# Kernel tuning notes

Measured on AMD Instinct MI355X. Metric: run time of the kernel, lower is better.

The kernel has to match this reference:

```python
import jax, jax.numpy as jnp
import numpy as np

B, T, D, H, K = 4, 2048, 512, 8, 31
INNER = 2048  # dim * ff_mult
DH = D // H   # 64
EPS = 1e-5

def _ln(x, g, b):
    m = jnp.mean(x, axis=-1, keepdims=True)
    v = jnp.var(x, axis=-1, keepdims=True)
    return (x - m) * jax.lax.rsqrt(v + EPS) * g + b

def _ff(x, g, b, w1, b1, w2, b2):
    h = jax.nn.silu(_ln(x, g, b) @ w1 + b1)
    return h @ w2 + b2

def _rope_cos_sin(t, dh, theta=10000.0):
    freqs = 1.0 / theta ** (jnp.arange(0, dh, 2, dtype=jnp.float32) / dh)
    ang = jnp.arange(t, dtype=jnp.float32)[:, None] * freqs[None, :]
    return jnp.cos(ang), jnp.sin(ang)

def _rotate(x, cos, sin):
    # x: [B,T,H,DH]; complex rotation on (even, odd) pairs, matches torch view_as_complex
    xr = x.reshape(x.shape[:-1] + (DH // 2, 2))
    xe, xo = xr[..., 0], xr[..., 1]
    c, s = cos[None, :, None, :], sin[None, :, None, :]
    return jnp.stack([xe * c - xo * s, xe * s + xo * c], axis=-1).reshape(x.shape)

def setup_inputs():
    ks = iter(jax.random.split(jax.random.key(0), 16))
    w = lambda *s: jax.random.normal(next(ks), s, jnp.float32) * 0.02
    ones = lambda n: jnp.ones((n,), jnp.float32)
    zeros = lambda n: jnp.zeros((n,), jnp.float32)
    return dict(
        x=jax.random.normal(next(ks), (B, T, D), jnp.float32),
        ff1_lng=ones(D), ff1_lnb=zeros(D),
        ff1_w1=w(D, INNER), ff1_b1=zeros(INNER), ff1_w2=w(INNER, D), ff1_b2=zeros(D),
        attn_lng=ones(D), attn_lnb=zeros(D),
        wq=w(D, D), wk=w(D, D), wv=w(D, D), wo=w(D, D),
        conv_lng=ones(D), conv_lnb=zeros(D),
        pw1_w=w(D, 2 * D), pw1_b=zeros(2 * D),
        dw_w=w(D, K), dw_b=zeros(D),
        bn_g=ones(D), bn_b=zeros(D),
        pw2_w=w(D, D), pw2_b=zeros(D),
        ff2_lng=ones(D), ff2_lnb=zeros(D),
        ff2_w1=w(D, INNER), ff2_b1=zeros(INNER), ff2_w2=w(INNER, D), ff2_b2=zeros(D),
        out_lng=ones(D), out_lnb=zeros(D),
    )

def reference(x, ff1_lng, ff1_lnb, ff1_w1, ff1_b1, ff1_w2, ff1_b2,
              attn_lng, attn_lnb, wq, wk, wv, wo,
              conv_lng, conv_lnb, pw1_w, pw1_b, dw_w, dw_b, bn_g, bn_b, pw2_w, pw2_b,
              ff2_lng, ff2_lnb, ff2_w1, ff2_b1, ff2_w2, ff2_b2,
              out_lng, out_lnb):
    # ff1 half-step
    x = x + 0.5 * _ff(x, ff1_lng, ff1_lnb, ff1_w1, ff1_b1, ff1_w2, ff1_b2)
    # RoPE MHSA
    h = _ln(x, attn_lng, attn_lnb)
    q = (h @ wq).reshape(B, T, H, DH)
    k = (h @ wk).reshape(B, T, H, DH)
    v = (h @ wv).reshape(B, T, H, DH)
    cos, sin = _rope_cos_sin(T, DH)
    q, k = _rotate(q, cos, sin), _rotate(k, cos, sin)
    scores = jnp.einsum('bqhd,bkhd->bhqk', q, k) / np.float32(np.sqrt(DH))
    o = jnp.einsum('bhqk,bkhd->bqhd', jax.nn.softmax(scores, axis=-1), v).reshape(B, T, D)
    x = x + o @ wo
    # Conformer conv module
    h = _ln(x, conv_lng, conv_lnb) @ pw1_w + pw1_b         # pointwise1 -> [B,T,2D]
    h = h[..., :D] * jax.nn.sigmoid(h[..., D:])            # GLU over channels
    h = h.transpose(0, 2, 1)                               # [B,D,T]
    h = jax.lax.conv_general_dilated(h, dw_w[:, None, :], (1,), [(K // 2, K // 2)],
                                     dimension_numbers=('NCH', 'OIH', 'NCH'),
                                     feature_group_count=D) + dw_b[None, :, None]
    mu = jnp.mean(h, axis=(0, 2), keepdims=True)           # training-mode BatchNorm1d
    var = jnp.var(h, axis=(0, 2), keepdims=True)
    h = (h - mu) * jax.lax.rsqrt(var + EPS) * bn_g[None, :, None] + bn_b[None, :, None]
    h = jax.nn.silu(h).transpose(0, 2, 1) @ pw2_w + pw2_b  # pointwise2 -> [B,T,D]
    x = x + h
    # ff2 half-step + final LN
    x = x + 0.5 * _ff(x, ff2_lng, ff2_lnb, ff2_w1, ff2_b1, ff2_w2, ff2_b2)
    return _ln(x, out_lng, out_lnb)
```

## Files before the change

kernel.cpp:

```cpp
#include <hip/hip_runtime.h>


typedef float  f32x4   __attribute__((ext_vector_type(4)));
typedef float  f32x16  __attribute__((ext_vector_type(16)));
typedef __bf16 bf16_t;
typedef __bf16 bf16x8  __attribute__((ext_vector_type(8)));
typedef unsigned short u16;
typedef unsigned short u16x4 __attribute__((ext_vector_type(4)));
typedef unsigned short u16x8 __attribute__((ext_vector_type(8)));
typedef unsigned int   u32x4 __attribute__((ext_vector_type(4)));

#define DEVI __device__ __forceinline__

static constexpr int CB = 4, CT = 2048, CD = 512, CH = 8, CDH = 64, CINNER = 2048, CK = 31;
static constexpr int CBT = CB * CT;

DEVI u16 f2bf(float f) {
  unsigned u = __builtin_bit_cast(unsigned, f);
  u += 0x7FFFu + ((u >> 16) & 1u);
  return (u16)(u >> 16);
}
DEVI float bf2f(u16 h) { return __builtin_bit_cast(float, (unsigned)h << 16); }
DEVI float sigm(float x) { return 1.0f / (1.0f + __expf(-x)); }

#if defined(__has_builtin)
#if __has_builtin(__builtin_amdgcn_exp2f)
#define FEX2(x) __builtin_amdgcn_exp2f(x)
#endif
#endif
#ifndef FEX2
DEVI float fex2_asm(float x) {
  float r;
  asm("v_exp_f32 %0, %1\n\ts_nop 1" : "=v"(r) : "v"(x));
  return r;
}
#define FEX2(x) fex2_asm(x)
#endif

DEVI unsigned cvtpk(float lo, float hi) {
  unsigned r;
  asm("v_cvt_pk_bf16_f32 %0, %1, %2" : "=v"(r) : "v"(lo), "v"(hi));
  return r;
}

DEVI void gload16(const bf16_t* g, bf16_t* l) {
  __builtin_amdgcn_global_load_lds(
      (const __attribute__((address_space(1))) unsigned int*)g,
      (__attribute__((address_space(3))) unsigned int*)l, 16, 0, 0);
}

DEVI void pipe_wait(int t, int nt) {
  if (t + 3 <= nt)      asm volatile("s_waitcnt vmcnt(12)" ::: "memory");
  else if (t + 2 == nt) asm volatile("s_waitcnt vmcnt(6)" ::: "memory");
  else                  asm volatile("s_waitcnt vmcnt(0)" ::: "memory");
}

enum { EPI_BF = 0, EPI_SILU_BF = 1, EPI_RES = 2, EPI_GLU = 3, EPI_QKV = 4, EPI_RESF = 5 };

template<int EPI>
__global__ __launch_bounds__(512) void gemm8(
    const bf16_t* __restrict__ A, const bf16_t* __restrict__ B,
    const float* __restrict__ bias, const float* __restrict__ res,
    void* __restrict__ Cv,
    int lda, int ldb, int ldc, int Kd, float scale)
{
  __shared__ __align__(16) bf16_t As[3][256 * 64];
  __shared__ __align__(16) bf16_t Bs[3][128 * 64];

  const int gx = gridDim.x;
  const int nwg = gx * gridDim.y;
  int wg = blockIdx.y * gx + blockIdx.x;
  wg = (wg & 7) * (nwg >> 3) + (wg >> 3);
  const int m0 = (wg / gx) * 256, n0 = (wg % gx) * 128;

  const int tid = threadIdx.x;
  const int wid = tid >> 6, lane = tid & 63;
  const int lrow = lane & 15, lk = lane >> 4;
  const int wm = (wid >> 1) * 64, wn = (wid & 1) * 64;
  const int r = tid >> 3;
  const int cs = (((tid & 7) ^ (r & 7)) << 3);
  const int fsw = lrow & 7;

  auto stage = [&](int kt, int s) {
    const bf16_t* ga = A + (long)(m0 + r) * lda + (kt * 64 + cs);
    const bf16_t* gb = B + (long)(n0 + r) * ldb + (kt * 64 + cs);
    bf16_t* as = &As[s][0];
    bf16_t* bs = &Bs[s][0];
#pragma unroll
    for (int it = 0; it < 4; ++it)
      gload16(ga + (long)it * 64 * lda, as + tid * 8 + it * 4096);
#pragma unroll
    for (int it = 0; it < 2; ++it)
      gload16(gb + (long)it * 64 * ldb, bs + tid * 8 + it * 4096);
  };

  f32x4 acc[4][4] = {};
  const int nt = Kd / 64;

  stage(0, 0);
  stage(1, 1);
  stage(2, 2);

  int s = 0;
  for (int t = 0; t < nt; ++t) {
    pipe_wait(t, nt);
    asm volatile("s_barrier" ::: "memory");

    bf16x8 av[2][4], bv[2][4];
    const bf16_t* as = &As[s][0];
    const bf16_t* bs = &Bs[s][0];
#pragma unroll
    for (int kk = 0; kk < 2; ++kk) {
#pragma unroll
      for (int i = 0; i < 4; ++i)
        av[kk][i] = *(const bf16x8*)&as[(wm + i * 16 + lrow) * 64 + ((((kk << 2) + lk) ^ fsw) << 3)];
#pragma unroll
      for (int j = 0; j < 4; ++j)
        bv[kk][j] = *(const bf16x8*)&bs[(wn + j * 16 + lrow) * 64 + ((((kk << 2) + lk) ^ fsw) << 3)];
    }
    __builtin_amdgcn_s_setprio(1);
#pragma unroll
    for (int kk = 0; kk < 2; ++kk)
#pragma unroll
      for (int i = 0; i < 4; ++i)
#pragma unroll
        for (int j = 0; j < 4; ++j)
          acc[i][j] = __builtin_amdgcn_mfma_f32_16x16x32_bf16(av[kk][i], bv[kk][j], acc[i][j], 0, 0, 0);
    __builtin_amdgcn_s_setprio(0);

    asm volatile("s_barrier" ::: "memory");
    if (t + 3 < nt) stage(t + 3, s);
    s = (s == 2) ? 0 : s + 1;
  }

  if constexpr (EPI == EPI_GLU) {
#pragma unroll
    for (int jp = 0; jp < 2; ++jp) {
      int oc = ((n0 + wn) >> 1) + jp * 16 + lrow;
      float ba = bias[oc], bb = bias[512 + oc];
#pragma unroll
      for (int i = 0; i < 4; ++i) {
#pragma unroll
        for (int rr = 0; rr < 4; ++rr) {
          int row = m0 + wm + i * 16 + lk * 4 + rr;
          float av_ = acc[i][2 * jp][rr] + ba;
          float bv_ = acc[i][2 * jp + 1][rr] + bb;
          ((bf16_t*)Cv)[(long)row * ldc + oc] = (bf16_t)(av_ * sigm(bv_));
        }
      }
    }
  } else if constexpr (EPI == EPI_QKV) {
    bf16_t* vt = (bf16_t*)res;
    const float2* cst = (const float2*)bias;
    const float SC = 0.125f * 1.44269504089f;
#pragma unroll
    for (int j = 0; j < 4; ++j) {
      int col = n0 + wn + j * 16 + lrow;
      if (col < 1024) {
        int ip = (col & 63) >> 1;
        bool odd = (col & 1) != 0;
        bool isQ = col < 512;
#pragma unroll
        for (int i = 0; i < 4; ++i) {
#pragma unroll
          for (int rr = 0; rr < 4; ++rr) {
            int row = m0 + wm + i * 16 + lk * 4 + rr;
            float2 csv = cst[(row & (CT - 1)) * 32 + ip];
            float mine = acc[i][j][rr];
            float other = __shfl_xor(mine, 1);
            float v = odd ? (other * csv.y + mine * csv.x)
                          : (mine * csv.x - other * csv.y);
            if (isQ) v *= SC;
            ((bf16_t*)Cv)[(long)row * ldc + col] = (bf16_t)v;
          }
        }
      } else {
        int dg = col - 1024;
        int hh = dg >> 6, d = dg & 63;
#pragma unroll
        for (int i = 0; i < 4; ++i) {
          int row0 = m0 + wm + i * 16 + lk * 4;
          int b = row0 >> 11, t = row0 & 2047;
          u16x4 pk;
#pragma unroll
          for (int rr = 0; rr < 4; ++rr) pk[rr] = f2bf(acc[i][j][rr]);
          *(u16x4*)(vt + ((long)(b * 8 + hh) * 64 + d) * 2048 + t) = pk;
        }
      }
    }
  } else {
#pragma unroll
    for (int j = 0; j < 4; ++j) {
      int col = n0 + wn + j * 16 + lrow;
      float bb = bias ? bias[col] : 0.0f;
#pragma unroll
      for (int i = 0; i < 4; ++i) {
#pragma unroll
        for (int rr = 0; rr < 4; ++rr) {
          int row = m0 + wm + i * 16 + lk * 4 + rr;
          long idx = (long)row * ldc + col;
          float v = (acc[i][j][rr] + bb) * scale;
          if constexpr (EPI == EPI_SILU_BF) v *= sigm(v);
          ((bf16_t*)Cv)[idx] = (bf16_t)v;
        }
      }
    }
  }
}

template<int BM, int BN, int BK, int EPI>
__global__ __launch_bounds__(256) void gemm_bf(
    const bf16_t* __restrict__ A, const bf16_t* __restrict__ B,
    const float* __restrict__ bias, const float* __restrict__ res,
    void* __restrict__ Cv,
    int lda, int ldb, int ldc, int Kd, float scale)
{
  __shared__ __align__(16) bf16_t As[BM * BK];
  __shared__ __align__(16) bf16_t Bs[BN * BK];

  const int gx = gridDim.x;
  const int nwg = gx * gridDim.y;
  int wg = blockIdx.y * gx + blockIdx.x;
  wg = (wg & 7) * (nwg >> 3) + (wg >> 3);
  const int m0 = (wg / gx) * BM, n0 = (wg % gx) * BN;

  const int tid = threadIdx.x;
  const int wid = tid >> 6, lane = tid & 63;
  const int lrow = lane & 15, lk = lane >> 4;
  constexpr int FM = BM / 32, FN = BN / 32;
  constexpr int NK = BK / 32;
  constexpr int TPR = BK / 8;
  constexpr int RPP = 256 / TPR;
  const int wm = (wid >> 1) * (BM / 2), wn = (wid & 1) * (BN / 2);
  const int r = tid / TPR;
  const int cs = (((tid & (TPR - 1)) ^ (r & 7)) << 3);
  const int fsw = lrow & 7;

  f32x4 acc[FM][FN] = {};

  for (int k0 = 0; k0 < Kd; k0 += BK) {
    const bf16_t* ga = A + (long)(m0 + r) * lda + (k0 + cs);
    const bf16_t* gb = B + (long)(n0 + r) * ldb + (k0 + cs);
#pragma unroll
    for (int it = 0; it < BM / RPP; ++it)
      gload16(ga + (long)it * RPP * lda, &As[tid * 8 + it * 2048]);
#pragma unroll
    for (int it = 0; it < BN / RPP; ++it)
      gload16(gb + (long)it * RPP * ldb, &Bs[tid * 8 + it * 2048]);
    __syncthreads();

    bf16x8 av[NK][FM], bv[NK][FN];
#pragma unroll
    for (int kk = 0; kk < NK; ++kk) {
#pragma unroll
      for (int i = 0; i < FM; ++i)
        av[kk][i] = *(const bf16x8*)&As[(wm + i * 16 + lrow) * BK + ((((kk << 2) + lk) ^ fsw) << 3)];
#pragma unroll
      for (int j = 0; j < FN; ++j)
        bv[kk][j] = *(const bf16x8*)&Bs[(wn + j * 16 + lrow) * BK + ((((kk << 2) + lk) ^ fsw) << 3)];
    }
#pragma unroll
    for (int kk = 0; kk < NK; ++kk)
#pragma unroll
      for (int i = 0; i < FM; ++i)
#pragma unroll
        for (int j = 0; j < FN; ++j)
          acc[i][j] = __builtin_amdgcn_mfma_f32_16x16x32_bf16(av[kk][i], bv[kk][j], acc[i][j], 0, 0, 0);
    __syncthreads();
  }

#pragma unroll
  for (int j = 0; j < FN; ++j) {
    int col = n0 + wn + j * 16 + lrow;
    float bb = bias ? bias[col] : 0.0f;
#pragma unroll
    for (int i = 0; i < FM; ++i) {
#pragma unroll
      for (int rr = 0; rr < 4; ++rr) {
        int row = m0 + wm + i * 16 + lk * 4 + rr;
        long idx = (long)row * ldc + col;
        float v = (acc[i][j][rr] + bb) * scale;
        if constexpr (EPI == EPI_SILU_BF) v *= sigm(v);
        if constexpr (EPI == EPI_RES) {
          ((bf16_t*)Cv)[idx] = (bf16_t)(bf2f(((const u16*)res)[idx]) + v);
        } else if constexpr (EPI == EPI_RESF) {
          ((bf16_t*)Cv)[idx] = (bf16_t)(res[idx] + v);
        } else {
          ((bf16_t*)Cv)[idx] = (bf16_t)v;
        }
      }
    }
  }
}

__global__ __launch_bounds__(256) void fattn_k(
    const bf16_t* __restrict__ QK,
    const bf16_t* __restrict__ VT,
    bf16_t* __restrict__ O)
{
  __shared__ __align__(16) bf16_t S[16384];

  const int tid = threadIdx.x;
  const int w = tid >> 6, lane = tid & 63;
  const int l31 = lane & 31, hi = lane >> 5;
  const int q0 = blockIdx.x * 128;
  const int bh = blockIdx.y, b = bh >> 3, h = bh & 7;

  const int r8 = tid >> 3;
  const int csw = ((tid & 7) ^ (r8 & 7)) << 3;
  const int fswl = l31 & 7;

  const bf16_t* Qg = QK + ((long)b * CT + q0) * 1536 + h * 64;
  const bf16_t* Kg = QK + (long)b * CT * 1536 + 512 + h * 64;
  const bf16_t* Vg = VT + (long)bh * 64 * 2048;

#pragma unroll
  for (int it = 0; it < 4; ++it)
    gload16(Qg + (long)(r8 + it * 32) * 1536 + csw, &S[8192 + tid * 8 + it * 2048]);
#pragma unroll
  for (int it = 0; it < 2; ++it)
    gload16(Kg + (long)(r8 + it * 32) * 1536 + csw, &S[tid * 8 + it * 2048]);
#pragma unroll
  for (int it = 0; it < 2; ++it)
    gload16(Vg + (long)(r8 + it * 32) * 2048 + csw, &S[4096 + tid * 8 + it * 2048]);
  __syncthreads();

  bf16x8 qb[4];
#pragma unroll
  for (int m = 0; m < 4; ++m)
    qb[m] = *(const bf16x8*)&S[8192 + (w * 32 + l31) * 64 + (((m * 2 + hi) ^ fswl) << 3)];
  __syncthreads();

  const u16x8 onesu = {0x3F80, 0x3F80, 0x3F80, 0x3F80, 0x3F80, 0x3F80, 0x3F80, 0x3F80};
  const bf16x8 onesf = __builtin_bit_cast(bf16x8, onesu);

  f32x16 o0 = {}, o1 = {}, lacc = {};

#define FA_BODY(CURK, CURV, NXTK, NXTV, KV0, STG)                               \
  {                                                                             \
    if (STG) {                                                                  \
      const int nxt = (KV0) + 64;                                               \
      _Pragma("unroll")                                                         \
      for (int it = 0; it < 2; ++it)                                            \
        gload16(Kg + (long)(nxt + r8 + it * 32) * 1536 + csw,                   \
                &S[(NXTK) + tid * 8 + it * 2048]);                              \
      _Pragma("unroll")                                                         \
      for (int it = 0; it < 2; ++it)                                            \
        gload16(Vg + (long)(r8 + it * 32) * 2048 + nxt + csw,                   \
                &S[(NXTV) + tid * 8 + it * 2048]);                              \
    }                                                                           \
    bf16x8 ka[2][4];                                                            \
    _Pragma("unroll")                                                           \
    for (int j = 0; j < 2; ++j)                                                 \
      _Pragma("unroll")                                                         \
      for (int m = 0; m < 4; ++m)                                               \
        ka[j][m] = *(const bf16x8*)&S[(CURK) + (j * 32 + l31) * 64 +            \
                                      (((m * 2 + hi) ^ fswl) << 3)];            \
    f32x16 s0 = {}, s1 = {};                                                    \
    __builtin_amdgcn_s_setprio(1);                                              \
    _Pragma("unroll")                                                           \
    for (int m = 0; m < 4; ++m) {                                               \
      s0 = __builtin_amdgcn_mfma_f32_32x32x16_bf16(ka[0][m], qb[m], s0, 0, 0, 0); \
      s1 = __builtin_amdgcn_mfma_f32_32x32x16_bf16(ka[1][m], qb[m], s1, 0, 0, 0); \
    }                                                                           \
    __builtin_amdgcn_s_setprio(0);                                              \
    _Pragma("unroll")                                                           \
    for (int rr = 0; rr < 16; ++rr) s0[rr] = FEX2(s0[rr]);                      \
    _Pragma("unroll")                                                           \
    for (int rr = 0; rr < 16; ++rr) s1[rr] = FEX2(s1[rr]);                      \
    bf16x8 pw[4];                                                               \
    _Pragma("unroll")                                                           \
    for (int jk = 0; jk < 4; ++jk) {                                            \
      float e0, e1, e2, e3, e4, e5, e6, e7;                                     \
      if (jk == 0) { e0=s0[0];e1=s0[1];e2=s0[2];e3=s0[3];e4=s0[4];e5=s0[5];e6=s0[6];e7=s0[7]; }        \
      else if (jk == 1) { e0=s0[8];e1=s0[9];e2=s0[10];e3=s0[11];e4=s0[12];e5=s0[13];e6=s0[14];e7=s0[15]; } \
      else if (jk == 2) { e0=s1[0];e1=s1[1];e2=s1[2];e3=s1[3];e4=s1[4];e5=s1[5];e6=s1[6];e7=s1[7]; }   \
      else { e0=s1[8];e1=s1[9];e2=s1[10];e3=s1[11];e4=s1[12];e5=s1[13];e6=s1[14];e7=s1[15]; }          \
      unsigned a0 = cvtpk(e0, e1), a1 = cvtpk(e2, e3);                          \
      unsigned b0 = cvtpk(e4, e5), b1 = cvtpk(e6, e7);                          \
      asm("v_permlane32_swap_b32 %0, %1" : "+v"(a0), "+v"(b0));                 \
      asm("v_permlane32_swap_b32 %0, %1" : "+v"(a1), "+v"(b1));                 \
      u32x4 t; t[0] = a0; t[1] = a1; t[2] = b0; t[3] = b1;                      \
      pw[jk] = __builtin_bit_cast(bf16x8, t);                                   \
    }                                                                           \
    bf16x8 va[2][4];                                                            \
    _Pragma("unroll")                                                           \
    for (int n = 0; n < 2; ++n)                                                 \
      _Pragma("unroll")                                                         \
      for (int jk = 0; jk < 4; ++jk)                                            \
        va[n][jk] = *(const bf16x8*)&S[(CURV) + (n * 32 + l31) * 64 +           \
                                       (((jk * 2 + hi) ^ fswl) << 3)];          \
    __builtin_amdgcn_s_setprio(1);                                              \
    _Pragma("unroll")                                                           \
    for (int jk = 0; jk < 4; ++jk) {                                            \
      o0 = __builtin_amdgcn_mfma_f32_32x32x16_bf16(va[0][jk], pw[jk], o0, 0, 0, 0); \
      o1 = __builtin_amdgcn_mfma_f32_32x32x16_bf16(va[1][jk], pw[jk], o1, 0, 0, 0); \
      lacc = __builtin_amdgcn_mfma_f32_32x32x16_bf16(onesf, pw[jk], lacc, 0, 0, 0); \
    }                                                                           \
    __builtin_amdgcn_s_setprio(0);                                              \
    __syncthreads();                                                            \
  }

  for (int kv0 = 0; kv0 < CT; kv0 += 128) {
    FA_BODY(0, 4096, 8192, 12288, kv0, 1)
    FA_BODY(8192, 12288, 0, 4096, kv0 + 64, (kv0 + 128 < CT))
  }
#undef FA_BODY

  float rl = 1.0f / lacc[0];
  bf16_t* Op = O + ((long)b * CT + q0 + w * 32 + l31) * CD + h * 64;
#pragma unroll
  for (int n = 0; n < 2; ++n) {
#pragma unroll
    for (int m = 0; m < 4; ++m) {
      u16x4 pk4;
#pragma unroll
      for (int e = 0; e < 4; ++e)
        pk4[e] = f2bf((n ? o1[m * 4 + e] : o0[m * 4 + e]) * rl);
      *(u16x4*)(Op + n * 32 + m * 8 + hi * 4) = pk4;
    }
  }
}

DEVI void wtrans_dev(const float* w, u16* o, int Kd, int N, int bx, int by,
                     int tid, u16 (*lt)[72])
{
  const int k0 = by * 64, n0 = bx * 64;
#pragma unroll
  for (int it = 0; it < 4; ++it) {
    int kk = (tid >> 4) + it * 16, nn = (tid & 15) * 4;
    float4 f = *(const float4*)(w + (long)(k0 + kk) * N + n0 + nn);
    lt[kk][nn + 0] = f2bf(f.x); lt[kk][nn + 1] = f2bf(f.y);
    lt[kk][nn + 2] = f2bf(f.z); lt[kk][nn + 3] = f2bf(f.w);
  }
  __syncthreads();
#pragma unroll
  for (int it = 0; it < 2; ++it) {
    int nn = (tid >> 3) + it * 32, kk = (tid & 7) * 8;
    u16x8 pk;
#pragma unroll
    for (int e = 0; e < 8; ++e) pk[e] = lt[kk + e][nn];
    *(u16x8*)(o + (long)(n0 + nn) * Kd + k0 + kk) = pk;
  }
}

DEVI void pwtrans_dev(const float* w, u16* o, int bx, int by, int tid,
                      u16 (*lt)[72])
{
  const int k0 = by * 64, n0 = bx * 64;
#pragma unroll
  for (int it = 0; it < 4; ++it) {
    int kk = (tid >> 4) + it * 16, nn = (tid & 15) * 4;
    float4 f = *(const float4*)(w + (long)(k0 + kk) * 1024 + n0 + nn);
    lt[kk][nn + 0] = f2bf(f.x); lt[kk][nn + 1] = f2bf(f.y);
    lt[kk][nn + 2] = f2bf(f.z); lt[kk][nn + 3] = f2bf(f.w);
  }
  __syncthreads();
#pragma unroll
  for (int it = 0; it < 2; ++it) {
    int nn = (tid >> 3) + it * 32, kk = (tid & 7) * 8;
    int s = n0 + nn;
    int d = ((s & 511) >> 4) * 32 + (s >> 9) * 16 + (s & 15);
    u16x8 pk;
#pragma unroll
    for (int e = 0; e < 8; ++e) pk[e] = lt[kk + e][nn];
    *(u16x8*)(o + (long)d * 512 + k0 + kk) = pk;
  }
}

__global__ __launch_bounds__(256) void prep_k(
    const float* ff1_w1, const float* ff1_w2,
    const float* wq, const float* wk, const float* wv, const float* wo,
    const float* pw1_w, const float* pw2_w,
    const float* ff2_w1, const float* ff2_w2, const float* dw_w,
    u16* w_ff1a, u16* w_ff1b, u16* w_qkv, u16* w_o, u16* w_pw1, u16* w_pw2,
    u16* w_ff2a, u16* w_ff2b, float* dwT, float2* ropeT)
{
  __shared__ u16 lt[64][72];
  const int r = blockIdx.x;
  const int tid = threadIdx.x;

  if (r < 256) {
    wtrans_dev(ff1_w1, w_ff1a, 512, 2048, r & 31, r >> 5, tid, lt);
  } else if (r < 512) {
    int r2 = r - 256;
    wtrans_dev(ff1_w2, w_ff1b, 2048, 512, r2 & 7, r2 >> 3, tid, lt);
  } else if (r < 576) {
    int r2 = r - 512;
    wtrans_dev(wq, w_qkv, 512, 512, r2 & 7, r2 >> 3, tid, lt);
  } else if (r < 640) {
    int r2 = r - 576;
    wtrans_dev(wk, w_qkv + (size_t)512 * 512, 512, 512, r2 & 7, r2 >> 3, tid, lt);
  } else if (r < 704) {
    int r2 = r - 640;
    wtrans_dev(wv, w_qkv + (size_t)1024 * 512, 512, 512, r2 & 7, r2 >> 3, tid, lt);
  } else if (r < 768) {
    int r2 = r - 704;
    wtrans_dev(wo, w_o, 512, 512, r2 & 7, r2 >> 3, tid, lt);
  } else if (r < 896) {
    int r2 = r - 768;
    pwtrans_dev(pw1_w, w_pw1, r2 & 15, r2 >> 4, tid, lt);
  } else if (r < 960) {
    int r2 = r - 896;
    wtrans_dev(pw2_w, w_pw2, 512, 512, r2 & 7, r2 >> 3, tid, lt);
  } else if (r < 1216) {
    int r2 = r - 960;
    wtrans_dev(ff2_w1, w_ff2a, 512, 2048, r2 & 31, r2 >> 5, tid, lt);
  } else if (r < 1472) {
    int r2 = r - 1216;
    wtrans_dev(ff2_w2, w_ff2b, 2048, 512, r2 & 7, r2 >> 3, tid, lt);
  } else if (r < 1534) {
    int i = (r - 1472) * 256 + tid;
    if (i < 512 * 31) { int c = i / 31, k = i % 31; dwT[k * 512 + c] = dw_w[i]; }
  } else {
    int i = (r - 1534) * 256 + tid;
    int t = i >> 5, ip = i & 31;
    float freq = __expf(-(float)ip * (9.210340371976184f / 32.0f));
    float ang = (float)t * freq;
    ropeT[i] = make_float2(cosf(ang), sinf(ang));
  }
}

template<int IBF, int OBF>
__global__ __launch_bounds__(256) void ln_k(
    const void* __restrict__ in, const float* __restrict__ g,
    const float* __restrict__ b, void* __restrict__ out)
{
  __shared__ float rs[4], rq[4];
  const long row = blockIdx.x;
  const int tid = threadIdx.x;
  float vx, vy;
  if (IBF) {
    unsigned u = ((const unsigned*)in)[row * 256 + tid];
    vx = bf2f((u16)u); vy = bf2f((u16)(u >> 16));
  } else {
    float2 v = ((const float2*)in)[row * 256 + tid];
    vx = v.x; vy = v.y;
  }
  float s = vx + vy, q = vx * vx + vy * vy;
#pragma unroll
  for (int o = 32; o; o >>= 1) { s += __shfl_xor(s, o); q += __shfl_xor(q, o); }
  if ((tid & 63) == 0) { rs[tid >> 6] = s; rq[tid >> 6] = q; }
  __syncthreads();
  s = rs[0] + rs[1] + rs[2] + rs[3];
  q = rq[0] + rq[1] + rq[2] + rq[3];
  float mean = s * (1.0f / CD);
  float var = q * (1.0f / CD) - mean * mean;
  float rstd = rsqrtf(var + 1e-5f);
  float2 gg = ((const float2*)g)[tid];
  float2 bb = ((const float2*)b)[tid];
  float ox = (vx - mean) * rstd * gg.x + bb.x;
  float oy = (vy - mean) * rstd * gg.y + bb.y;
  if (OBF) {
    unsigned pk = ((unsigned)f2bf(oy) << 16) | f2bf(ox);
    ((unsigned*)out)[row * 256 + tid] = pk;
  } else {
    ((float2*)out)[row * 256 + tid] = make_float2(ox, oy);
  }
}

__global__ __launch_bounds__(256) void dwconv_k(
    const u16* __restrict__ in, const float* __restrict__ wT,
    const float* __restrict__ wb, u16* __restrict__ out)
{
  long idx = (long)blockIdx.x * 256 + threadIdx.x;
  int c4 = (int)(idx & 127) * 4;
  int t0 = (int)((idx >> 7) & 255) * 8;
  int b = (int)(idx >> 15);
  const u16* base = in + (long)b * CT * CD;
  float4 bias = *(const float4*)(wb + c4);
  float4 acc[8];
#pragma unroll
  for (int t = 0; t < 8; ++t) acc[t] = bias;
#pragma unroll
  for (int j = 0; j < 38; ++j) {
    int tr = t0 + j - 15;
    float4 row = make_float4(0.f, 0.f, 0.f, 0.f);
    if (tr >= 0 && tr < CT) {
      u16x4 rv = *(const u16x4*)(base + (long)tr * CD + c4);
      row = make_float4(bf2f(rv[0]), bf2f(rv[1]), bf2f(rv[2]), bf2f(rv[3]));
    }
#pragma unroll
    for (int t = 0; t < 8; ++t) {
      int k = j - t;
      if (k >= 0 && k < CK) {
        float4 w4 = *(const float4*)(wT + k * CD + c4);
        acc[t].x += row.x * w4.x; acc[t].y += row.y * w4.y;
        acc[t].z += row.z * w4.z; acc[t].w += row.w * w4.w;
      }
    }
  }
#pragma unroll
  for (int t = 0; t < 8; ++t) {
    u16x4 pk;
    pk[0] = f2bf(acc[t].x); pk[1] = f2bf(acc[t].y);
    pk[2] = f2bf(acc[t].z); pk[3] = f2bf(acc[t].w);
    *(u16x4*)(out + ((long)b * CT + t0 + t) * CD + c4) = pk;
  }
}

__global__ __launch_bounds__(256) void bn_part_k(
    const u16* __restrict__ in, float* __restrict__ psum, float* __restrict__ psq)
{
  const int blk = blockIdx.x;
  const int tid = threadIdx.x;
  const int c0 = tid, c1 = tid + 256;
  const int rows = CBT / 256;
  const u16* base = in + (long)blk * rows * CD;
  float s0 = 0, q0 = 0, s1 = 0, q1 = 0;
  for (int r = 0; r < rows; ++r) {
    float v0 = bf2f(base[(long)r * CD + c0]); s0 += v0; q0 += v0 * v0;
    float v1 = bf2f(base[(long)r * CD + c1]); s1 += v1; q1 += v1 * v1;
  }
  psum[blk * CD + c0] = s0; psq[blk * CD + c0] = q0;
  psum[blk * CD + c1] = s1; psq[blk * CD + c1] = q1;
}

__global__ __launch_bounds__(256) void bn_fin_k(
    const float* __restrict__ psum, const float* __restrict__ psq,
    float* __restrict__ stat)
{
  int c = blockIdx.x * 256 + threadIdx.x;
  float s = 0, q = 0;
  for (int i = 0; i < 256; ++i) { s += psum[i * CD + c]; q += psq[i * CD + c]; }
  float mean = s * (1.0f / CBT);
  float var = q * (1.0f / CBT) - mean * mean;
  stat[c] = mean;
  stat[CD + c] = rsqrtf(var + 1e-5f);
}

__global__ __launch_bounds__(256) void bn_app_k(
    const u16* __restrict__ h, const float* __restrict__ stat,
    const float* __restrict__ g, const float* __restrict__ b,
    u16* __restrict__ out)
{
  long idx = (long)blockIdx.x * 256 + threadIdx.x;
  int c = (int)(idx & 511);
  float v = (bf2f(h[idx]) - stat[c]) * stat[CD + c] * g[c] + b[c];
  v = v * sigm(v);
  out[idx] = f2bf(v);
}

extern "C" void kernel_launch(void* const* d_in, const int* in_sizes, int n_in,
                              void* d_out, int out_size, void* d_ws, size_t ws_size,
                              hipStream_t stream)
{
  const float* x        = (const float*)d_in[0];
  const float* ff1_lng  = (const float*)d_in[1];
  const float* ff1_lnb  = (const float*)d_in[2];
  const float* ff1_w1   = (const float*)d_in[3];
  const float* ff1_b1   = (const float*)d_in[4];
  const float* ff1_w2   = (const float*)d_in[5];
  const float* ff1_b2   = (const float*)d_in[6];
  const float* attn_lng = (const float*)d_in[7];
  const float* attn_lnb = (const float*)d_in[8];
  const float* wq       = (const float*)d_in[9];
  const float* wk       = (const float*)d_in[10];
  const float* wv       = (const float*)d_in[11];
  const float* wo       = (const float*)d_in[12];
  const float* conv_lng = (const float*)d_in[13];
  const float* conv_lnb = (const float*)d_in[14];
  const float* pw1_w    = (const float*)d_in[15];
  const float* pw1_b    = (const float*)d_in[16];
  const float* dw_w     = (const float*)d_in[17];
  const float* dw_b     = (const float*)d_in[18];
  const float* bn_g     = (const float*)d_in[19];
  const float* bn_b     = (const float*)d_in[20];
  const float* pw2_w    = (const float*)d_in[21];
  const float* pw2_b    = (const float*)d_in[22];
  const float* ff2_lng  = (const float*)d_in[23];
  const float* ff2_lnb  = (const float*)d_in[24];
  const float* ff2_w1   = (const float*)d_in[25];
  const float* ff2_b1   = (const float*)d_in[26];
  const float* ff2_w2   = (const float*)d_in[27];
  const float* ff2_b2   = (const float*)d_in[28];
  const float* out_lng  = (const float*)d_in[29];
  const float* out_lnb  = (const float*)d_in[30];
  float* out = (float*)d_out;

  char* p = (char*)d_ws;
  auto alloc = [&](size_t bytes) { char* r = p; p += (bytes + 255) & ~(size_t)255; return r; };
  bf16_t* bufX   = (bf16_t*)alloc((size_t)CBT * CD * 2);
  bf16_t* bufH   = (bf16_t*)alloc((size_t)CBT * CD * 2);
  bf16_t* bufQKV = (bf16_t*)alloc((size_t)CBT * 1536 * 2);
  bf16_t* bufO   = (bf16_t*)alloc((size_t)CBT * CD * 2);
  bf16_t* bufVT  = (bf16_t*)alloc((size_t)CBT * CD * 2);
  bf16_t* bufP   = (bf16_t*)alloc((size_t)CBT * CINNER * 2);
  bf16_t* w_ff1a = (bf16_t*)alloc((size_t)CD * CINNER * 2);
  bf16_t* w_ff1b = (bf16_t*)alloc((size_t)CD * CINNER * 2);
  bf16_t* w_qkv  = (bf16_t*)alloc((size_t)CD * 1536 * 2);
  bf16_t* w_o    = (bf16_t*)alloc((size_t)CD * CD * 2);
  bf16_t* w_pw1  = (bf16_t*)alloc((size_t)CD * 2 * CD * 2);
  bf16_t* w_pw2  = (bf16_t*)alloc((size_t)CD * CD * 2);
  bf16_t* w_ff2a = (bf16_t*)alloc((size_t)CD * CINNER * 2);
  bf16_t* w_ff2b = (bf16_t*)alloc((size_t)CD * CINNER * 2);
  float* dwT  = (float*)alloc((size_t)CK * CD * 4);
  float2* ropeT = (float2*)alloc((size_t)CT * 32 * 8);
  float* psum = (float*)alloc((size_t)256 * CD * 4);
  float* psq  = (float*)alloc((size_t)256 * CD * 4);
  float* stat = (float*)alloc((size_t)2 * CD * 4);

  const dim3 blk(256);
  const dim3 blk8(512);

  prep_k<<<dim3(1790), blk, 0, stream>>>(
      ff1_w1, ff1_w2, wq, wk, wv, wo, pw1_w, pw2_w, ff2_w1, ff2_w2, dw_w,
      (u16*)w_ff1a, (u16*)w_ff1b, (u16*)w_qkv, (u16*)w_o, (u16*)w_pw1,
      (u16*)w_pw2, (u16*)w_ff2a, (u16*)w_ff2b, dwT, ropeT);

  ln_k<0, 1><<<dim3(CBT), blk, 0, stream>>>(x, ff1_lng, ff1_lnb, bufH);
  gemm8<EPI_SILU_BF><<<dim3(16, 32), blk8, 0, stream>>>(
      bufH, w_ff1a, ff1_b1, nullptr, bufP, CD, CD, CINNER, CD, 1.0f);
  gemm_bf<64, 128, 128, EPI_RESF><<<dim3(4, 128), blk, 0, stream>>>(
      bufP, w_ff1b, ff1_b2, x, bufX, CINNER, CINNER, CD, CINNER, 0.5f);

  ln_k<1, 1><<<dim3(CBT), blk, 0, stream>>>(bufX, attn_lng, attn_lnb, bufH);
  gemm8<EPI_QKV><<<dim3(12, 32), blk8, 0, stream>>>(
      bufH, w_qkv, (const float*)ropeT, (const float*)bufVT, bufQKV, CD, CD, 1536, CD, 1.0f);
  fattn_k<<<dim3(CT / 128, CB * CH), blk, 0, stream>>>(bufQKV, bufVT, bufO);
  gemm_bf<64, 128, 128, EPI_RES><<<dim3(4, 128), blk, 0, stream>>>(
      bufO, w_o, nullptr, (const float*)bufX, bufX, CD, CD, CD, CD, 1.0f);

  ln_k<1, 1><<<dim3(CBT), blk, 0, stream>>>(bufX, conv_lng, conv_lnb, bufH);
  gemm8<EPI_GLU><<<dim3(8, 32), blk8, 0, stream>>>(
      bufH, w_pw1, pw1_b, nullptr, bufH, CD, CD, CD, CD, 1.0f);
  dwconv_k<<<dim3(512), blk, 0, stream>>>((const u16*)bufH, dwT, dw_b, (u16*)bufO);
  bn_part_k<<<dim3(256), blk, 0, stream>>>((const u16*)bufO, psum, psq);
  bn_fin_k<<<dim3(2), blk, 0, stream>>>(psum, psq, stat);
  bn_app_k<<<dim3(CBT * CD / 256), blk, 0, stream>>>((const u16*)bufO, stat, bn_g, bn_b, (u16*)bufH);
  gemm_bf<64, 128, 128, EPI_RES><<<dim3(4, 128), blk, 0, stream>>>(
      bufH, w_pw2, pw2_b, (const float*)bufX, bufX, CD, CD, CD, CD, 1.0f);

  ln_k<1, 1><<<dim3(CBT), blk, 0, stream>>>(bufX, ff2_lng, ff2_lnb, bufH);
  gemm8<EPI_SILU_BF><<<dim3(16, 32), blk8, 0, stream>>>(
      bufH, w_ff2a, ff2_b1, nullptr, bufP, CD, CD, CINNER, CD, 1.0f);
  gemm_bf<64, 128, 128, EPI_RES><<<dim3(4, 128), blk, 0, stream>>>(
      bufP, w_ff2b, ff2_b2, (const float*)bufX, bufX, CINNER, CINNER, CD, CINNER, 0.5f);

  ln_k<1, 0><<<dim3(CBT), blk, 0, stream>>>(bufX, out_lng, out_lnb, out);

  (void)in_sizes; (void)n_in; (void)out_size; (void)ws_size;
}
```

Baseline: 339.6 us.

## Widen attention blocks to 256 queries and use one wave per LayerNorm row

```diff
diff --git a/kernel.cpp b/kernel.cpp
--- a/kernel.cpp
+++ b/kernel.cpp
@@ -293,17 +293,17 @@
   }
 }
 
-__global__ __launch_bounds__(256) void fattn_k(
+__global__ __launch_bounds__(512) void fattn_k(
     const bf16_t* __restrict__ QK,
     const bf16_t* __restrict__ VT,
     bf16_t* __restrict__ O)
 {
-  __shared__ __align__(16) bf16_t S[16384];
+  __shared__ __align__(16) bf16_t S[32768];
 
   const int tid = threadIdx.x;
   const int w = tid >> 6, lane = tid & 63;
   const int l31 = lane & 31, hi = lane >> 5;
-  const int q0 = blockIdx.x * 128;
+  const int q0 = blockIdx.x * 256;
   const int bh = blockIdx.y, b = bh >> 3, h = bh & 7;
 
   const int r8 = tid >> 3;
@@ -316,20 +316,15 @@
 
 #pragma unroll
   for (int it = 0; it < 4; ++it)
-    gload16(Qg + (long)(r8 + it * 32) * 1536 + csw, &S[8192 + tid * 8 + it * 2048]);
-#pragma unroll
-  for (int it = 0; it < 2; ++it)
-    gload16(Kg + (long)(r8 + it * 32) * 1536 + csw, &S[tid * 8 + it * 2048]);
-#pragma unroll
-  for (int it = 0; it < 2; ++it)
-    gload16(Vg + (long)(r8 + it * 32) * 2048 + csw, &S[4096 + tid * 8 + it * 2048]);
+    gload16(Qg + (long)(r8 + it * 64) * 1536 + csw, &S[16384 + tid * 8 + it * 4096]);
+  gload16(Kg + (long)r8 * 1536 + csw, &S[tid * 8]);
+  gload16(Vg + (long)r8 * 2048 + csw, &S[4096 + tid * 8]);
   __syncthreads();
 
   bf16x8 qb[4];
 #pragma unroll
   for (int m = 0; m < 4; ++m)
-    qb[m] = *(const bf16x8*)&S[8192 + (w * 32 + l31) * 64 + (((m * 2 + hi) ^ fswl) << 3)];
-  __syncthreads();
+    qb[m] = *(const bf16x8*)&S[16384 + (w * 32 + l31) * 64 + (((m * 2 + hi) ^ fswl) << 3)];
 
   const u16x8 onesu = {0x3F80, 0x3F80, 0x3F80, 0x3F80, 0x3F80, 0x3F80, 0x3F80, 0x3F80};
   const bf16x8 onesf = __builtin_bit_cast(bf16x8, onesu);
@@ -340,14 +335,8 @@
   {                                                                             \
     if (STG) {                                                                  \
       const int nxt = (KV0) + 64;                                               \
-      _Pragma("unroll")                                                         \
-      for (int it = 0; it < 2; ++it)                                            \
-        gload16(Kg + (long)(nxt + r8 + it * 32) * 1536 + csw,                   \
-                &S[(NXTK) + tid * 8 + it * 2048]);                              \
-      _Pragma("unroll")                                                         \
-      for (int it = 0; it < 2; ++it)                                            \
-        gload16(Vg + (long)(r8 + it * 32) * 2048 + nxt + csw,                   \
-                &S[(NXTV) + tid * 8 + it * 2048]);                              \
+      gload16(Kg + (long)(nxt + r8) * 1536 + csw, &S[(NXTK) + tid * 8]);        \
+      gload16(Vg + (long)r8 * 2048 + nxt + csw, &S[(NXTV) + tid * 8]);          \
     }                                                                           \
     bf16x8 ka[2][4];                                                            \
     _Pragma("unroll")                                                           \
@@ -526,36 +515,42 @@
     const void* __restrict__ in, const float* __restrict__ g,
     const float* __restrict__ b, void* __restrict__ out)
 {
-  __shared__ float rs[4], rq[4];
-  const long row = blockIdx.x;
-  const int tid = threadIdx.x;
-  float vx, vy;
+  const int w = threadIdx.x >> 6, lane = threadIdx.x & 63;
+  const long row = (long)blockIdx.x * 4 + w;
+  float v[8];
   if (IBF) {
-    unsigned u = ((const unsigned*)in)[row * 256 + tid];
-    vx = bf2f((u16)u); vy = bf2f((u16)(u >> 16));
+    u16x8 u = ((const u16x8*)in)[row * 64 + lane];
+#pragma unroll
+    for (int e = 0; e < 8; ++e) v[e] = bf2f(u[e]);
   } else {
-    float2 v = ((const float2*)in)[row * 256 + tid];
-    vx = v.x; vy = v.y;
-  }
-  float s = vx + vy, q = vx * vx + vy * vy;
+    float4 f0 = ((const float4*)in)[row * 128 + lane * 2];
+    float4 f1 = ((const float4*)in)[row * 128 + lane * 2 + 1];
+    v[0] = f0.x; v[1] = f0.y; v[2] = f0.z; v[3] = f0.w;
+    v[4] = f1.x; v[5] = f1.y; v[6] = f1.z; v[7] = f1.w;
+  }
+  float s = 0, q = 0;
+#pragma unroll
+  for (int e = 0; e < 8; ++e) { s += v[e]; q += v[e] * v[e]; }
 #pragma unroll
   for (int o = 32; o; o >>= 1) { s += __shfl_xor(s, o); q += __shfl_xor(q, o); }
-  if ((tid & 63) == 0) { rs[tid >> 6] = s; rq[tid >> 6] = q; }
-  __syncthreads();
-  s = rs[0] + rs[1] + rs[2] + rs[3];
-  q = rq[0] + rq[1] + rq[2] + rq[3];
   float mean = s * (1.0f / CD);
   float var = q * (1.0f / CD) - mean * mean;
   float rstd = rsqrtf(var + 1e-5f);
-  float2 gg = ((const float2*)g)[tid];
-  float2 bb = ((const float2*)b)[tid];
-  float ox = (vx - mean) * rstd * gg.x + bb.x;
-  float oy = (vy - mean) * rstd * gg.y + bb.y;
+  float4 g0 = ((const float4*)g)[lane * 2], g1 = ((const float4*)g)[lane * 2 + 1];
+  float4 b0 = ((const float4*)b)[lane * 2], b1 = ((const float4*)b)[lane * 2 + 1];
+  float gg[8] = {g0.x, g0.y, g0.z, g0.w, g1.x, g1.y, g1.z, g1.w};
+  float bb[8] = {b0.x, b0.y, b0.z, b0.w, b1.x, b1.y, b1.z, b1.w};
+  float o8[8];
+#pragma unroll
+  for (int e = 0; e < 8; ++e) o8[e] = (v[e] - mean) * rstd * gg[e] + bb[e];
   if (OBF) {
-    unsigned pk = ((unsigned)f2bf(oy) << 16) | f2bf(ox);
-    ((unsigned*)out)[row * 256 + tid] = pk;
+    u16x8 pk;
+#pragma unroll
+    for (int e = 0; e < 8; ++e) pk[e] = f2bf(o8[e]);
+    ((u16x8*)out)[row * 64 + lane] = pk;
   } else {
-    ((float2*)out)[row * 256 + tid] = make_float2(ox, oy);
+    ((float4*)out)[row * 128 + lane * 2] = make_float4(o8[0], o8[1], o8[2], o8[3]);
+    ((float4*)out)[row * 128 + lane * 2 + 1] = make_float4(o8[4], o8[5], o8[6], o8[7]);
   }
 }
 
@@ -708,20 +703,20 @@
       (u16*)w_ff1a, (u16*)w_ff1b, (u16*)w_qkv, (u16*)w_o, (u16*)w_pw1,
       (u16*)w_pw2, (u16*)w_ff2a, (u16*)w_ff2b, dwT, ropeT);
 
-  ln_k<0, 1><<<dim3(CBT), blk, 0, stream>>>(x, ff1_lng, ff1_lnb, bufH);
+  ln_k<0, 1><<<dim3(CBT / 4), blk, 0, stream>>>(x, ff1_lng, ff1_lnb, bufH);
   gemm8<EPI_SILU_BF><<<dim3(16, 32), blk8, 0, stream>>>(
       bufH, w_ff1a, ff1_b1, nullptr, bufP, CD, CD, CINNER, CD, 1.0f);
   gemm_bf<64, 128, 128, EPI_RESF><<<dim3(4, 128), blk, 0, stream>>>(
       bufP, w_ff1b, ff1_b2, x, bufX, CINNER, CINNER, CD, CINNER, 0.5f);
 
-  ln_k<1, 1><<<dim3(CBT), blk, 0, stream>>>(bufX, attn_lng, attn_lnb, bufH);
+  ln_k<1, 1><<<dim3(CBT / 4), blk, 0, stream>>>(bufX, attn_lng, attn_lnb, bufH);
   gemm8<EPI_QKV><<<dim3(12, 32), blk8, 0, stream>>>(
       bufH, w_qkv, (const float*)ropeT, (const float*)bufVT, bufQKV, CD, CD, 1536, CD, 1.0f);
-  fattn_k<<<dim3(CT / 128, CB * CH), blk, 0, stream>>>(bufQKV, bufVT, bufO);
+  fattn_k<<<dim3(CT / 256, CB * CH), blk8, 0, stream>>>(bufQKV, bufVT, bufO);
   gemm_bf<64, 128, 128, EPI_RES><<<dim3(4, 128), blk, 0, stream>>>(
       bufO, w_o, nullptr, (const float*)bufX, bufX, CD, CD, CD, CD, 1.0f);
 
-  ln_k<1, 1><<<dim3(CBT), blk, 0, stream>>>(bufX, conv_lng, conv_lnb, bufH);
+  ln_k<1, 1><<<dim3(CBT / 4), blk, 0, stream>>>(bufX, conv_lng, conv_lnb, bufH);
   gemm8<EPI_GLU><<<dim3(8, 32), blk8, 0, stream>>>(
       bufH, w_pw1, pw1_b, nullptr, bufH, CD, CD, CD, CD, 1.0f);
   dwconv_k<<<dim3(512), blk, 0, stream>>>((const u16*)bufH, dwT, dw_b, (u16*)bufO);
@@ -731,13 +726,13 @@
   gemm_bf<64, 128, 128, EPI_RES><<<dim3(4, 128), blk, 0, stream>>>(
       bufH, w_pw2, pw2_b, (const float*)bufX, bufX, CD, CD, CD, CD, 1.0f);
 
-  ln_k<1, 1><<<dim3(CBT), blk, 0, stream>>>(bufX, ff2_lng, ff2_lnb, bufH);
+  ln_k<1, 1><<<dim3(CBT / 4), blk, 0, stream>>>(bufX, ff2_lng, ff2_lnb, bufH);
   gemm8<EPI_SILU_BF><<<dim3(16, 32), blk8, 0, stream>>>(
       bufH, w_ff2a, ff2_b1, nullptr, bufP, CD, CD, CINNER, CD, 1.0f);
   gemm_bf<64, 128, 128, EPI_RES><<<dim3(4, 128), blk, 0, stream>>>(
       bufP, w_ff2b, ff2_b2, (const float*)bufX, bufX, CINNER, CINNER, CD, CINNER, 0.5f);
 
-  ln_k<1, 0><<<dim3(CBT), blk, 0, stream>>>(bufX, out_lng, out_lnb, out);
+  ln_k<1, 0><<<dim3(CBT / 4), blk, 0, stream>>>(bufX, out_lng, out_lnb, out);
 
   (void)in_sizes; (void)n_in; (void)out_size; (void)ws_size;
 }
```

Result: faster. 322.7 us (-5.0%).
